# Kernel tuning notes

Hardware: AMD Instinct MI355X
Metric: run time of the kernel (lower is better)

Reference implementation:

```python
import jax, jax.numpy as jnp
import numpy as np

B, M, K, E, V, HOPS = 256, 128, 4, 512, 32000, 3


def setup_inputs() -> dict:
    key = jax.random.key(0)
    ks = jax.random.split(key, 12)

    def emb_table(k):
        t = 0.1 * jax.random.normal(k, (V, E), dtype=jnp.float32)
        return t.at[0].set(0.0)  # padding_idx=0

    inp = {
        "context": jax.random.randint(ks[0], (B, M, K), 0, V),
        "y_": jax.random.randint(ks[1], (B,), 0, V),
        "h_": jax.random.normal(ks[2], (1, B, E), dtype=jnp.float32),
        # embedding tables; C[i] tied to A[i+1], so distinct: A0,A1,A2,C2
        "A0": emb_table(ks[3]),
        "A1": emb_table(ks[4]),
        "A2": emb_table(ks[5]),
        "C2": emb_table(ks[6]),
        # GRU (single layer, single step): PyTorch layout [3E, E] and [3E]
        "W_ih": 0.05 * jax.random.normal(ks[7], (3 * E, E), dtype=jnp.float32),
        "W_hh": 0.05 * jax.random.normal(ks[8], (3 * E, E), dtype=jnp.float32),
        "b_ih": jnp.zeros((3 * E,), dtype=jnp.float32),
        "b_hh": jnp.zeros((3 * E,), dtype=jnp.float32),
        # lin_vocab: Linear(2E -> V)
        "lin_W": 0.02 * jax.random.normal(ks[9], (V, 2 * E), dtype=jnp.float32),
        "lin_b": jnp.zeros((V,), dtype=jnp.float32),
    }
    return inp


def _gru_step(x, h, W_ih, W_hh, b_ih, b_hh):
    gi = x @ W_ih.T + b_ih  # [B, 3E]
    gh = h @ W_hh.T + b_hh
    i_r, i_z, i_n = jnp.split(gi, 3, axis=-1)
    h_r, h_z, h_n = jnp.split(gh, 3, axis=-1)
    r = jax.nn.sigmoid(i_r + h_r)
    z = jax.nn.sigmoid(i_z + h_z)
    n = jnp.tanh(i_n + r * h_n)
    return (1.0 - z) * n + z * h


def reference(context, y_, h_, A0, A1, A2, C2, W_ih, W_hh, b_ih, b_hh, lin_W, lin_b):
    # memories[hop] = sum_k A[hop][context], memories[hops] = sum_k C[hops-1][context]
    tables = [A0, A1, A2, C2]
    memories = [t[context].sum(axis=2) for t in tables]  # each [B, M, E]

    m = A1[y_]  # C[0](y_) -- C[0].weight tied to A[1].weight, [B, E]
    h = _gru_step(m, h_[0], W_ih, W_hh, b_ih, b_hh)  # [B, E]

    q = h
    p = None
    p_vocab = None
    for hop in range(HOPS):
        p = jnp.einsum("bme,be->bm", memories[hop], q)  # dot-attention scores
        attn = jax.nn.softmax(p, axis=1)
        o = jnp.einsum("bm,bme->be", attn, memories[hop + 1])
        if hop == 0:
            p_vocab = jnp.concatenate([q, o], axis=1) @ lin_W.T + lin_b  # [B, V]
        q = q + o

    p_ptr = p  # last hop's pre-softmax scores [B, M]
    return (p_ptr, p_vocab, h[None])  # h: [1, B, E]
```

## Files before the change

kernel.cpp:

```cpp
#include <hip/hip_runtime.h>
#include <hip/hip_bf16.h>
#include <stdint.h>
#include <stddef.h>

#define Bb 256
#define Mm 128
#define Ee 512
#define Vv 32000
#define E3 1536

typedef __attribute__((ext_vector_type(8))) short bf16x8;
typedef __attribute__((ext_vector_type(4))) float f32x4;

__device__ __forceinline__ float bf2f(unsigned short u) {
  union { unsigned int i; float f; } v; v.i = ((unsigned int)u) << 16; return v.f;
}
__device__ __forceinline__ unsigned int f2bf(float f) {
  union { float f; unsigned int u; } v; v.f = f;
  unsigned int u = v.u;
  return ((u + 0x7fffu + ((u >> 16) & 1u)) >> 16);
}

__global__ void convert_kernel(const float* __restrict__ A0, const float* __restrict__ A1,
                               const float* __restrict__ A2,
                               unsigned short* __restrict__ tabB) {
  const int t = blockIdx.y;
  const float* src = (t == 0) ? A0 : (t == 1) ? A1 : A2;
  unsigned short* dst = tabB + (size_t)t * Vv * Ee;
  const int n4 = Vv * Ee / 4;
  for (int i = blockIdx.x * blockDim.x + threadIdx.x; i < n4; i += gridDim.x * blockDim.x) {
    f32x4 v = __builtin_nontemporal_load((const f32x4*)src + i);
    unsigned int o0 = f2bf(v.x) | (f2bf(v.y) << 16);
    unsigned int o1 = f2bf(v.z) | (f2bf(v.w) << 16);
    ((uint2*)dst)[i] = make_uint2(o0, o1);
  }
}

__global__ void gru_gemm_kernel(const int* __restrict__ y,
                                const float* __restrict__ A1,
                                const float* __restrict__ hprev,
                                const float* __restrict__ W_ih,
                                const float* __restrict__ W_hh,
                                float* __restrict__ gi,
                                float* __restrict__ gh) {
  const int z = blockIdx.z;
  const float* W = z ? W_hh : W_ih;
  float* C = z ? gh : gi;
  const int by = blockIdx.x * 64;
  const int jy = blockIdx.y * 64;
  __shared__ float As[16][65];
  __shared__ float Bs[16][65];
  const int tx = threadIdx.x & 15, ty = threadIdx.x >> 4;
  float acc[4][4] = {};
  for (int k0 = 0; k0 < Ee; k0 += 16) {
#pragma unroll
    for (int it = 0; it < 4; ++it) {
      int r = ty + it * 16;
      int row = by + r;
      const float* arow = z ? (hprev + (size_t)row * Ee) : (A1 + (size_t)y[row] * Ee);
      As[tx][r] = arow[k0 + tx];
      Bs[tx][r] = W[(size_t)(jy + r) * Ee + k0 + tx];
    }
    __syncthreads();
#pragma unroll
    for (int kk = 0; kk < 16; ++kk) {
      float a[4], bb[4];
#pragma unroll
      for (int i = 0; i < 4; ++i) { a[i] = As[kk][ty * 4 + i]; bb[i] = Bs[kk][tx * 4 + i]; }
#pragma unroll
      for (int i = 0; i < 4; ++i)
#pragma unroll
        for (int j = 0; j < 4; ++j)
          acc[i][j] += a[i] * bb[j];
    }
    __syncthreads();
  }
#pragma unroll
  for (int i = 0; i < 4; ++i)
#pragma unroll
    for (int j = 0; j < 4; ++j)
      C[(size_t)(by + ty * 4 + i) * E3 + jy + tx * 4 + j] = acc[i][j];
}

__global__ __launch_bounds__(1024) void fused_kernel(
    const int* __restrict__ ctx,
    const unsigned short* __restrict__ tabB,
    const float* __restrict__ A0, const float* __restrict__ A1,
    const float* __restrict__ A2,
    const float* __restrict__ gi, const float* __restrict__ gh,
    const float* __restrict__ b_ih, const float* __restrict__ b_hh,
    const float* __restrict__ h0,
    float* __restrict__ out_h, unsigned short* __restrict__ in2,
    float* __restrict__ p_out) {
  extern __shared__ char smem[];
  unsigned short* Vlds = (unsigned short*)smem;
  float* p_lds = (float*)(smem + 131072);
  float* qbuf = (float*)(smem + 131584);
  float* obuf = (float*)(smem + 133632);

  const int b = blockIdx.x;
  const int tid = threadIdx.x;
  const int lane = tid & 63, w = tid >> 6;

  if (tid < 512) {
    const int e = tid;
    const float* gib = gi + (size_t)b * E3;
    const float* ghb = gh + (size_t)b * E3;
    float ir = gib[e] + b_ih[e];
    float iz = gib[512 + e] + b_ih[512 + e];
    float inn = gib[1024 + e] + b_ih[1024 + e];
    float hr = ghb[e] + b_hh[e];
    float hz = ghb[512 + e] + b_hh[512 + e];
    float hn = ghb[1024 + e] + b_hh[1024 + e];
    float r = 1.f / (1.f + __expf(-(ir + hr)));
    float z = 1.f / (1.f + __expf(-(iz + hz)));
    float n = tanhf(inn + r * hn);
    float hp = h0[(size_t)b * Ee + e];
    float hnew = (1.f - z) * n + z * hp;
    out_h[(size_t)b * Ee + e] = hnew;
    in2[(size_t)b * 1024 + e] = (unsigned short)f2bf(hnew);
    qbuf[e] = hnew;
  }

#define GATHER_B(T)                                                          \
  {                                                                          \
    const unsigned short* Tb = tabB + (size_t)(T) * ((size_t)Vv * Ee);       \
    _Pragma("unroll 2")                                                      \
    for (int r8 = 0; r8 < 8; ++r8) {                                         \
      const int row = w * 8 + r8;                                            \
      const int4 cc = *(const int4*)(ctx + ((size_t)b * Mm + row) * 4);      \
      uint4 va = *(const uint4*)(Tb + (size_t)cc.x * Ee + lane * 8);         \
      uint4 vb = *(const uint4*)(Tb + (size_t)cc.y * Ee + lane * 8);         \
      uint4 vc = *(const uint4*)(Tb + (size_t)cc.z * Ee + lane * 8);         \
      uint4 vd = *(const uint4*)(Tb + (size_t)cc.w * Ee + lane * 8);         \
      const unsigned int* pa = (const unsigned int*)&va;                     \
      const unsigned int* pb = (const unsigned int*)&vb;                     \
      const unsigned int* pc = (const unsigned int*)&vc;                     \
      const unsigned int* pd = (const unsigned int*)&vd;                     \
      unsigned int o[4];                                                     \
      _Pragma("unroll")                                                      \
      for (int j = 0; j < 4; ++j) {                                          \
        float lo = bf2f((unsigned short)(pa[j] & 0xffff)) +                  \
                   bf2f((unsigned short)(pb[j] & 0xffff)) +                  \
                   bf2f((unsigned short)(pc[j] & 0xffff)) +                  \
                   bf2f((unsigned short)(pd[j] & 0xffff));                   \
        float hi = bf2f((unsigned short)(pa[j] >> 16)) +                     \
                   bf2f((unsigned short)(pb[j] >> 16)) +                     \
                   bf2f((unsigned short)(pc[j] >> 16)) +                     \
                   bf2f((unsigned short)(pd[j] >> 16));                      \
        o[j] = f2bf(lo) | (f2bf(hi) << 16);                                  \
      }                                                                      \
      *(uint4*)(Vlds + (size_t)row * Ee + lane * 8) = *(uint4*)o;            \
    }                                                                        \
  }

#define GATHER_F(TAB)                                                        \
  {                                                                          \
    _Pragma("unroll 2")                                                      \
    for (int r8 = 0; r8 < 8; ++r8) {                                         \
      const int row = w * 8 + r8;                                            \
      const int4 cc = *(const int4*)(ctx + ((size_t)b * Mm + row) * 4);      \
      const float* s0 = TAB + (size_t)cc.x * Ee + lane * 8;                  \
      const float* s1 = TAB + (size_t)cc.y * Ee + lane * 8;                  \
      const float* s2 = TAB + (size_t)cc.z * Ee + lane * 8;                  \
      const float* s3 = TAB + (size_t)cc.w * Ee + lane * 8;                  \
      float4 a0 = *(const float4*)s0, a1 = *(const float4*)(s0 + 4);         \
      float4 b0 = *(const float4*)s1, b1 = *(const float4*)(s1 + 4);         \
      float4 c0 = *(const float4*)s2, c1 = *(const float4*)(s2 + 4);         \
      float4 d0 = *(const float4*)s3, d1 = *(const float4*)(s3 + 4);         \
      unsigned int o[4];                                                     \
      o[0] = f2bf(a0.x + b0.x + c0.x + d0.x) |                               \
             (f2bf(a0.y + b0.y + c0.y + d0.y) << 16);                        \
      o[1] = f2bf(a0.z + b0.z + c0.z + d0.z) |                               \
             (f2bf(a0.w + b0.w + c0.w + d0.w) << 16);                        \
      o[2] = f2bf(a1.x + b1.x + c1.x + d1.x) |                               \
             (f2bf(a1.y + b1.y + c1.y + d1.y) << 16);                        \
      o[3] = f2bf(a1.z + b1.z + c1.z + d1.z) |                               \
             (f2bf(a1.w + b1.w + c1.w + d1.w) << 16);                        \
      *(uint4*)(Vlds + (size_t)row * Ee + lane * 8) = *(uint4*)o;            \
    }                                                                        \
  }

#define GATHER(T, TAB) { if (tabB) GATHER_B(T) else GATHER_F(TAB) }

#define SCORE_PHASE(EMIT)                                                    \
  {                                                                          \
    float qf[8];                                                             \
    *(float4*)&qf[0] = *(const float4*)&qbuf[lane * 8];                      \
    *(float4*)&qf[4] = *(const float4*)&qbuf[lane * 8 + 4];                  \
    _Pragma("unroll")                                                        \
    for (int r = 0; r < 8; ++r) {                                            \
      const int m = w * 8 + r;                                               \
      uint4 kv = *(const uint4*)(Vlds + (size_t)m * Ee + lane * 8);          \
      const unsigned int* p4 = (const unsigned int*)&kv;                     \
      float s = 0.f;                                                         \
      _Pragma("unroll")                                                      \
      for (int x = 0; x < 4; ++x) {                                          \
        s += bf2f((unsigned short)(p4[x] & 0xffff)) * qf[2 * x];             \
        s += bf2f((unsigned short)(p4[x] >> 16)) * qf[2 * x + 1];            \
      }                                                                      \
      _Pragma("unroll")                                                      \
      for (int off = 32; off > 0; off >>= 1) s += __shfl_down(s, off);       \
      if (lane == 0) { EMIT; }                                               \
    }                                                                        \
  }

#define SOFTMAX_PHASE                                                        \
  if (tid < 64) {                                                            \
    float v0 = p_lds[tid], v1 = p_lds[tid + 64];                             \
    float mx = fmaxf(v0, v1);                                                \
    _Pragma("unroll")                                                        \
    for (int off = 32; off > 0; off >>= 1) mx = fmaxf(mx, __shfl_xor(mx, off)); \
    float e0 = __expf(v0 - mx), e1 = __expf(v1 - mx);                        \
    float s = e0 + e1;                                                       \
    _Pragma("unroll")                                                        \
    for (int off = 32; off > 0; off >>= 1) s += __shfl_xor(s, off);          \
    float inv = 1.f / s;                                                     \
    p_lds[tid] = e0 * inv;                                                   \
    p_lds[tid + 64] = e1 * inv;                                              \
  }

#define O_PHASE                                                              \
  {                                                                          \
    const int g = tid >> 8, t = tid & 255;                                   \
    const int e2 = t * 2;                                                    \
    float a0 = 0.f, a1 = 0.f;                                                \
    _Pragma("unroll 4")                                                      \
    for (int m = g * 32; m < g * 32 + 32; ++m) {                             \
      unsigned int vv = *(const unsigned int*)(Vlds + (size_t)m * Ee + e2);  \
      float ww = p_lds[m];                                                   \
      a0 += ww * bf2f((unsigned short)(vv & 0xffff));                        \
      a1 += ww * bf2f((unsigned short)(vv >> 16));                           \
    }                                                                        \
    obuf[g * 512 + e2] = a0;                                                 \
    obuf[g * 512 + e2 + 1] = a1;                                             \
  }

  GATHER(0, A0)
  __syncthreads();
  SCORE_PHASE(p_lds[m] = s)
  __syncthreads();
  SOFTMAX_PHASE
  GATHER(1, A1)
  __syncthreads();
  O_PHASE
  __syncthreads();
  if (tid < 512) {
    const int e = tid;
    float o = obuf[e] + obuf[512 + e] + obuf[1024 + e] + obuf[1536 + e];
    qbuf[e] = qbuf[e] + o;
    in2[(size_t)b * 1024 + 512 + e] = (unsigned short)f2bf(o);
  }
  __syncthreads();

  SCORE_PHASE(p_lds[m] = s)
  __syncthreads();
  SOFTMAX_PHASE
  GATHER(2, A2)
  __syncthreads();
  O_PHASE
  __syncthreads();
  if (tid < 512) {
    const int e = tid;
    qbuf[e] = qbuf[e] + obuf[e] + obuf[512 + e] + obuf[1024 + e] + obuf[1536 + e];
  }
  __syncthreads();

  SCORE_PHASE(p_out[b * Mm + m] = s)
}

__global__ __launch_bounds__(512) void pvocab_kernel(
    const unsigned short* __restrict__ in2,
    const float* __restrict__ lin_W,
    const float* __restrict__ lin_b,
    float* __restrict__ out_pv) {
  const int v0 = blockIdx.x * 128;
  const int m0 = blockIdx.y * 128;
  const int tid = threadIdx.x;
  const int lane = tid & 63, w = tid >> 6;
  const int wm = w >> 2, wn = w & 3;
  const int l15 = lane & 15, lg = lane >> 4;
  __shared__ __align__(16) unsigned short As[2][128][64];
  __shared__ __align__(16) unsigned short Ws[2][128][64];

  const int au = tid & 7, arb = tid >> 3;
  const int wc = tid & 15, wrb = tid >> 4;

  f32x4 acc[4][2];
#pragma unroll
  for (int i = 0; i < 4; ++i)
#pragma unroll
    for (int j = 0; j < 2; ++j)
      acc[i][j] = (f32x4){0.f, 0.f, 0.f, 0.f};

  uint4 aR[2];
  float4 wR[4];

#define PV_STAGE_LOAD(K0)                                                    \
  {                                                                          \
    _Pragma("unroll")                                                        \
    for (int it = 0; it < 2; ++it) {                                         \
      int r = arb + it * 64;                                                 \
      aR[it] = *(const uint4*)(in2 + (size_t)(m0 + r) * 1024 + (K0) + au * 8); \
    }                                                                        \
    _Pragma("unroll")                                                        \
    for (int it = 0; it < 4; ++it) {                                         \
      int r = wrb + it * 32;                                                 \
      wR[it] = *(const float4*)(lin_W + (size_t)(v0 + r) * 1024 + (K0) + wc * 4); \
    }                                                                        \
  }

#define PV_STAGE_WRITE(BUF)                                                  \
  {                                                                          \
    _Pragma("unroll")                                                        \
    for (int it = 0; it < 2; ++it) {                                         \
      int r = arb + it * 64;                                                 \
      *(uint4*)(&As[BUF][r][((au + r) & 7) * 8]) = aR[it];                   \
    }                                                                        \
    _Pragma("unroll")                                                        \
    for (int it = 0; it < 4; ++it) {                                         \
      int r = wrb + it * 32;                                                 \
      unsigned int o0 = f2bf(wR[it].x) | (f2bf(wR[it].y) << 16);             \
      unsigned int o1 = f2bf(wR[it].z) | (f2bf(wR[it].w) << 16);             \
      int u = wc >> 1, h = wc & 1;                                           \
      *(uint2*)(&Ws[BUF][r][((u + r) & 7) * 8 + h * 4]) = make_uint2(o0, o1); \
    }                                                                        \
  }

  PV_STAGE_LOAD(0)
  PV_STAGE_WRITE(0)
  __syncthreads();

  int cur = 0;
  for (int t = 0; t < 16; ++t) {
    if (t + 1 < 16) PV_STAGE_LOAD((t + 1) * 64)
#pragma unroll
    for (int kk = 0; kk < 2; ++kk) {
      const int cu = kk * 4 + lg;
      bf16x8 wf[2], af[4];
#pragma unroll
      for (int j = 0; j < 2; ++j) {
        int row = wn * 32 + j * 16 + l15;
        wf[j] = *(const bf16x8*)(&Ws[cur][row][((cu + row) & 7) * 8]);
      }
#pragma unroll
      for (int i = 0; i < 4; ++i) {
        int row = wm * 64 + i * 16 + l15;
        af[i] = *(const bf16x8*)(&As[cur][row][((cu + row) & 7) * 8]);
      }
#pragma unroll
      for (int i = 0; i < 4; ++i)
#pragma unroll
        for (int j = 0; j < 2; ++j)
          acc[i][j] = __builtin_amdgcn_mfma_f32_16x16x32_bf16(af[i], wf[j], acc[i][j], 0, 0, 0);
    }
    if (t + 1 < 16) {
      PV_STAGE_WRITE(cur ^ 1)
      __syncthreads();
      cur ^= 1;
    }
  }

#pragma unroll
  for (int j = 0; j < 2; ++j) {
    int v = v0 + wn * 32 + j * 16 + l15;
    float bias = lin_b[v];
#pragma unroll
    for (int i = 0; i < 4; ++i) {
      int brow = m0 + wm * 64 + i * 16 + lg * 4;
#pragma unroll
      for (int rr = 0; rr < 4; ++rr)
        out_pv[(size_t)(brow + rr) * Vv + v] = acc[i][j][rr] + bias;
    }
  }
}

extern "C" void kernel_launch(void* const* d_in, const int* in_sizes, int n_in,
                              void* d_out, int out_size, void* d_ws, size_t ws_size,
                              hipStream_t stream) {
  const int* ctx = (const int*)d_in[0];
  const int* y = (const int*)d_in[1];
  const float* h0 = (const float*)d_in[2];
  const float* A0 = (const float*)d_in[3];
  const float* A1 = (const float*)d_in[4];
  const float* A2 = (const float*)d_in[5];
  const float* W_ih = (const float*)d_in[7];
  const float* W_hh = (const float*)d_in[8];
  const float* b_ih = (const float*)d_in[9];
  const float* b_hh = (const float*)d_in[10];
  const float* lin_W = (const float*)d_in[11];
  const float* lin_b = (const float*)d_in[12];

  const size_t tabBytes = (size_t)3 * Vv * Ee * 2;
  const size_t giBytes = (size_t)Bb * E3 * 4;
  const size_t in2Bytes = (size_t)Bb * 1024 * 2;
  const bool bf16path = ws_size >= tabBytes + 2 * giBytes + in2Bytes;

  char* ws = (char*)d_ws;
  size_t off = 0;
  unsigned short* tabB = nullptr;
  if (bf16path) { tabB = (unsigned short*)ws; off += tabBytes; }
  float* gi = (float*)(ws + off); off += giBytes;
  float* gh = (float*)(ws + off); off += giBytes;
  unsigned short* in2 = (unsigned short*)(ws + off);

  float* out = (float*)d_out;
  float* p_ptr = out;
  float* p_voc = out + Bb * Mm;
  float* out_h = out + Bb * Mm + (size_t)Bb * Vv;

  if (bf16path)
    convert_kernel<<<dim3(4096, 3), 256, 0, stream>>>(A0, A1, A2, tabB);
  gru_gemm_kernel<<<dim3(4, 24, 2), 256, 0, stream>>>(y, A1, h0, W_ih, W_hh, gi, gh);
  hipFuncSetAttribute((const void*)fused_kernel,
                      hipFuncAttributeMaxDynamicSharedMemorySize, 141824);
  fused_kernel<<<Bb, 1024, 141824, stream>>>(ctx, tabB, A0, A1, A2, gi, gh,
                                             b_ih, b_hh, h0, out_h, in2, p_ptr);
  pvocab_kernel<<<dim3(Vv / 128, 2), 512, 0, stream>>>(in2, lin_W, lin_b, p_voc);
}
```

Baseline: 220.4 us.

## Retile p_vocab GEMM to 64-row blocks with A fragments read from global

Restructures the vocabulary projection kernel into 256-thread blocks covering 64 batch rows by 128 vocab columns, with the batch dimension on grid x so neighbouring blocks share the same lin_W tile through cache. The activation operand is no longer staged in shared memory; each wave loads its bf16 MFMA fragments straight from global memory. Only the converted weight tile is double-buffered in LDS. This cuts LDS use and staging work and gives more blocks, but lin_W is now read and converted by four blocks instead of two, and the uncoalesced global A-fragment loads inside the MFMA loop may add latency.

Result: slower. 348.1 us (+57.9%).

```diff
diff --git a/kernel.cpp b/kernel.cpp
--- a/kernel.cpp
+++ b/kernel.cpp
@@ -269,21 +269,19 @@
   SCORE_PHASE(p_out[b * Mm + m] = s)
 }
 
-__global__ __launch_bounds__(512) void pvocab_kernel(
+__global__ __launch_bounds__(256) void pvocab_kernel(
     const unsigned short* __restrict__ in2,
     const float* __restrict__ lin_W,
     const float* __restrict__ lin_b,
     float* __restrict__ out_pv) {
-  const int v0 = blockIdx.x * 128;
-  const int m0 = blockIdx.y * 128;
+  const int m0 = blockIdx.x * 64;
+  const int v0 = blockIdx.y * 128;
   const int tid = threadIdx.x;
-  const int lane = tid & 63, w = tid >> 6;
-  const int wm = w >> 2, wn = w & 3;
+  const int lane = tid & 63, wn = tid >> 6;
   const int l15 = lane & 15, lg = lane >> 4;
-  __shared__ __align__(16) unsigned short As[2][128][64];
+  const int n_base = v0 + wn * 32;
   __shared__ __align__(16) unsigned short Ws[2][128][64];
 
-  const int au = tid & 7, arb = tid >> 3;
   const int wc = tid & 15, wrb = tid >> 4;
 
   f32x4 acc[4][2];
@@ -293,33 +291,22 @@
     for (int j = 0; j < 2; ++j)
       acc[i][j] = (f32x4){0.f, 0.f, 0.f, 0.f};
 
-  uint4 aR[2];
-  float4 wR[4];
+  float4 wR[8];
 
 #define PV_STAGE_LOAD(K0)                                                    \
   {                                                                          \
     _Pragma("unroll")                                                        \
-    for (int it = 0; it < 2; ++it) {                                         \
-      int r = arb + it * 64;                                                 \
-      aR[it] = *(const uint4*)(in2 + (size_t)(m0 + r) * 1024 + (K0) + au * 8); \
-    }                                                                        \
+    for (int it = 0; it < 8; ++it) {                                         \
+      int r = wrb + it * 16;                                                 \
+      wR[it] = *(const float4*)(lin_W + (size_t)(v0 + r) * 1024 + (K0) + wc * 4); \
+    }                                                                        \
+  }
+
+#define PV_STAGE_WRITE(BUF)                                                  \
+  {                                                                          \
     _Pragma("unroll")                                                        \
-    for (int it = 0; it < 4; ++it) {                                         \
-      int r = wrb + it * 32;                                                 \
-      wR[it] = *(const float4*)(lin_W + (size_t)(v0 + r) * 1024 + (K0) + wc * 4); \
-    }                                                                        \
-  }
-
-#define PV_STAGE_WRITE(BUF)                                                  \
-  {                                                                          \
-    _Pragma("unroll")                                                        \
-    for (int it = 0; it < 2; ++it) {                                         \
-      int r = arb + it * 64;                                                 \
-      *(uint4*)(&As[BUF][r][((au + r) & 7) * 8]) = aR[it];                   \
-    }                                                                        \
-    _Pragma("unroll")                                                        \
-    for (int it = 0; it < 4; ++it) {                                         \
-      int r = wrb + it * 32;                                                 \
+    for (int it = 0; it < 8; ++it) {                                         \
+      int r = wrb + it * 16;                                                 \
       unsigned int o0 = f2bf(wR[it].x) | (f2bf(wR[it].y) << 16);             \
       unsigned int o1 = f2bf(wR[it].z) | (f2bf(wR[it].w) << 16);             \
       int u = wc >> 1, h = wc & 1;                                           \
@@ -337,6 +324,7 @@
 #pragma unroll
     for (int kk = 0; kk < 2; ++kk) {
       const int cu = kk * 4 + lg;
+      const int col = t * 64 + kk * 32 + lg * 8;
       bf16x8 wf[2], af[4];
 #pragma unroll
       for (int j = 0; j < 2; ++j) {
@@ -344,10 +332,8 @@
         wf[j] = *(const bf16x8*)(&Ws[cur][row][((cu + row) & 7) * 8]);
       }
 #pragma unroll
-      for (int i = 0; i < 4; ++i) {
-        int row = wm * 64 + i * 16 + l15;
-        af[i] = *(const bf16x8*)(&As[cur][row][((cu + row) & 7) * 8]);
-      }
+      for (int i = 0; i < 4; ++i)
+        af[i] = *(const bf16x8*)(in2 + (size_t)(m0 + i * 16 + l15) * 1024 + col);
 #pragma unroll
       for (int i = 0; i < 4; ++i)
 #pragma unroll
@@ -363,11 +349,11 @@
 
 #pragma unroll
   for (int j = 0; j < 2; ++j) {
-    int v = v0 + wn * 32 + j * 16 + l15;
+    int v = n_base + j * 16 + l15;
     float bias = lin_b[v];
 #pragma unroll
     for (int i = 0; i < 4; ++i) {
-      int brow = m0 + wm * 64 + i * 16 + lg * 4;
+      int brow = m0 + i * 16 + lg * 4;
 #pragma unroll
       for (int rr = 0; rr < 4; ++rr)
         out_pv[(size_t)(brow + rr) * Vv + v] = acc[i][j][rr] + bias;
@@ -416,5 +402,5 @@
                       hipFuncAttributeMaxDynamicSharedMemorySize, 141824);
   fused_kernel<<<Bb, 1024, 141824, stream>>>(ctx, tabB, A0, A1, A2, gi, gh,
                                              b_ih, b_hh, h0, out_h, in2, p_ptr);
-  pvocab_kernel<<<dim3(Vv / 128, 2), 512, 0, stream>>>(in2, lin_W, lin_b, p_voc);
-}
+  pvocab_kernel<<<dim3(4, Vv / 128), 256, 0, stream>>>(in2, lin_W, lin_b, p_voc);
+}
```

## Store activations in MFMA fragment layout and cover full batch per vocab tile

Applied to the files above, without the earlier changes.

The fused kernel now writes the bf16 [h, o] activations in a pre-swizzled layout that matches the MFMA A-fragment order. The vocab GEMM can then load A fragments straight from global memory instead of staging them through LDS. Each pvocab block now has 1024 threads and covers all 256 batch rows for its 128 vocab columns, so every lin_W tile is read and converted to bf16 once instead of twice. K-steps are widened to 128, which halves the number of barriers. The cost is per-MFMA global loads of activations, which rely on L2 hits, and fewer blocks (250) for the device's CUs.

New measurement: 218.6 us. No clear change (-0.8%).

```diff
diff --git a/kernel.cpp b/kernel.cpp
--- a/kernel.cpp
+++ b/kernel.cpp
@@ -20,6 +20,10 @@
   unsigned int u = v.u;
   return ((u + 0x7fffu + ((u >> 16) & 1u)) >> 16);
 }
+
+#define IN2F_IDX(bb, col)                                                     \
+  ((((size_t)((bb) >> 4) * 32 + ((col) >> 5)) * 512) +                        \
+   (size_t)((((bb) & 15) + (((col) >> 3) & 3) * 16) * 8 + ((col) & 7)))
 
 __global__ void convert_kernel(const float* __restrict__ A0, const float* __restrict__ A1,
                                const float* __restrict__ A2,
@@ -90,7 +94,7 @@
     const float* __restrict__ gi, const float* __restrict__ gh,
     const float* __restrict__ b_ih, const float* __restrict__ b_hh,
     const float* __restrict__ h0,
-    float* __restrict__ out_h, unsigned short* __restrict__ in2,
+    float* __restrict__ out_h, unsigned short* __restrict__ in2f,
     float* __restrict__ p_out) {
   extern __shared__ char smem[];
   unsigned short* Vlds = (unsigned short*)smem;
@@ -118,7 +122,7 @@
     float hp = h0[(size_t)b * Ee + e];
     float hnew = (1.f - z) * n + z * hp;
     out_h[(size_t)b * Ee + e] = hnew;
-    in2[(size_t)b * 1024 + e] = (unsigned short)f2bf(hnew);
+    in2f[IN2F_IDX(b, e)] = (unsigned short)f2bf(hnew);
     qbuf[e] = hnew;
   }
 
@@ -249,7 +253,7 @@
     const int e = tid;
     float o = obuf[e] + obuf[512 + e] + obuf[1024 + e] + obuf[1536 + e];
     qbuf[e] = qbuf[e] + o;
-    in2[(size_t)b * 1024 + 512 + e] = (unsigned short)f2bf(o);
+    in2f[IN2F_IDX(b, 512 + e)] = (unsigned short)f2bf(o);
   }
   __syncthreads();
 
@@ -269,22 +273,19 @@
   SCORE_PHASE(p_out[b * Mm + m] = s)
 }
 
-__global__ __launch_bounds__(512) void pvocab_kernel(
-    const unsigned short* __restrict__ in2,
+__global__ __launch_bounds__(1024) void pvocab_kernel(
+    const unsigned short* __restrict__ in2f,
     const float* __restrict__ lin_W,
     const float* __restrict__ lin_b,
     float* __restrict__ out_pv) {
   const int v0 = blockIdx.x * 128;
-  const int m0 = blockIdx.y * 128;
   const int tid = threadIdx.x;
   const int lane = tid & 63, w = tid >> 6;
   const int wm = w >> 2, wn = w & 3;
   const int l15 = lane & 15, lg = lane >> 4;
-  __shared__ __align__(16) unsigned short As[2][128][64];
-  __shared__ __align__(16) unsigned short Ws[2][128][64];
-
-  const int au = tid & 7, arb = tid >> 3;
-  const int wc = tid & 15, wrb = tid >> 4;
+  __shared__ __align__(16) unsigned short Ws[2][128][128];
+
+  const int wc = tid & 31, wrb = tid >> 5;
 
   f32x4 acc[4][2];
 #pragma unroll
@@ -293,37 +294,26 @@
     for (int j = 0; j < 2; ++j)
       acc[i][j] = (f32x4){0.f, 0.f, 0.f, 0.f};
 
-  uint4 aR[2];
   float4 wR[4];
 
-#define PV_STAGE_LOAD(K0)                                                    \
-  {                                                                          \
-    _Pragma("unroll")                                                        \
-    for (int it = 0; it < 2; ++it) {                                         \
-      int r = arb + it * 64;                                                 \
-      aR[it] = *(const uint4*)(in2 + (size_t)(m0 + r) * 1024 + (K0) + au * 8); \
-    }                                                                        \
+#define PV_STAGE_LOAD(T)                                                     \
+  {                                                                          \
     _Pragma("unroll")                                                        \
     for (int it = 0; it < 4; ++it) {                                         \
       int r = wrb + it * 32;                                                 \
-      wR[it] = *(const float4*)(lin_W + (size_t)(v0 + r) * 1024 + (K0) + wc * 4); \
+      wR[it] = *(const float4*)(lin_W + (size_t)(v0 + r) * 1024 + (T) * 128 + wc * 4); \
     }                                                                        \
   }
 
 #define PV_STAGE_WRITE(BUF)                                                  \
   {                                                                          \
-    _Pragma("unroll")                                                        \
-    for (int it = 0; it < 2; ++it) {                                         \
-      int r = arb + it * 64;                                                 \
-      *(uint4*)(&As[BUF][r][((au + r) & 7) * 8]) = aR[it];                   \
-    }                                                                        \
     _Pragma("unroll")                                                        \
     for (int it = 0; it < 4; ++it) {                                         \
       int r = wrb + it * 32;                                                 \
       unsigned int o0 = f2bf(wR[it].x) | (f2bf(wR[it].y) << 16);             \
       unsigned int o1 = f2bf(wR[it].z) | (f2bf(wR[it].w) << 16);             \
       int u = wc >> 1, h = wc & 1;                                           \
-      *(uint2*)(&Ws[BUF][r][((u + r) & 7) * 8 + h * 4]) = make_uint2(o0, o1); \
+      *(uint2*)(&Ws[BUF][r][((u + r) & 15) * 8 + h * 4]) = make_uint2(o0, o1); \
     }                                                                        \
   }
 
@@ -332,21 +322,21 @@
   __syncthreads();
 
   int cur = 0;
-  for (int t = 0; t < 16; ++t) {
-    if (t + 1 < 16) PV_STAGE_LOAD((t + 1) * 64)
-#pragma unroll
-    for (int kk = 0; kk < 2; ++kk) {
-      const int cu = kk * 4 + lg;
+  for (int t = 0; t < 8; ++t) {
+    if (t + 1 < 8) PV_STAGE_LOAD(t + 1)
+#pragma unroll
+    for (int kb4 = 0; kb4 < 4; ++kb4) {
+      const int kb = t * 4 + kb4;
       bf16x8 wf[2], af[4];
 #pragma unroll
       for (int j = 0; j < 2; ++j) {
         int row = wn * 32 + j * 16 + l15;
-        wf[j] = *(const bf16x8*)(&Ws[cur][row][((cu + row) & 7) * 8]);
+        wf[j] = *(const bf16x8*)(&Ws[cur][row][((kb4 * 4 + lg + row) & 15) * 8]);
       }
 #pragma unroll
       for (int i = 0; i < 4; ++i) {
-        int row = wm * 64 + i * 16 + l15;
-        af[i] = *(const bf16x8*)(&As[cur][row][((cu + row) & 7) * 8]);
+        int mblk = wm * 4 + i;
+        af[i] = *(const bf16x8*)(in2f + ((size_t)(mblk * 32 + kb)) * 512 + lane * 8);
       }
 #pragma unroll
       for (int i = 0; i < 4; ++i)
@@ -354,7 +344,7 @@
         for (int j = 0; j < 2; ++j)
           acc[i][j] = __builtin_amdgcn_mfma_f32_16x16x32_bf16(af[i], wf[j], acc[i][j], 0, 0, 0);
     }
-    if (t + 1 < 16) {
+    if (t + 1 < 8) {
       PV_STAGE_WRITE(cur ^ 1)
       __syncthreads();
       cur ^= 1;
@@ -367,7 +357,7 @@
     float bias = lin_b[v];
 #pragma unroll
     for (int i = 0; i < 4; ++i) {
-      int brow = m0 + wm * 64 + i * 16 + lg * 4;
+      int brow = wm * 64 + i * 16 + lg * 4;
 #pragma unroll
       for (int rr = 0; rr < 4; ++rr)
         out_pv[(size_t)(brow + rr) * Vv + v] = acc[i][j][rr] + bias;
@@ -402,7 +392,7 @@
   if (bf16path) { tabB = (unsigned short*)ws; off += tabBytes; }
   float* gi = (float*)(ws + off); off += giBytes;
   float* gh = (float*)(ws + off); off += giBytes;
-  unsigned short* in2 = (unsigned short*)(ws + off);
+  unsigned short* in2f = (unsigned short*)(ws + off);
 
   float* out = (float*)d_out;
   float* p_ptr = out;
@@ -415,6 +405,6 @@
   hipFuncSetAttribute((const void*)fused_kernel,
                       hipFuncAttributeMaxDynamicSharedMemorySize, 141824);
   fused_kernel<<<Bb, 1024, 141824, stream>>>(ctx, tabB, A0, A1, A2, gi, gh,
-                                             b_ih, b_hh, h0, out_h, in2, p_ptr);
-  pvocab_kernel<<<dim3(Vv / 128, 2), 512, 0, stream>>>(in2, lin_W, lin_b, p_voc);
-}
+                                             b_ih, b_hh, h0, out_h, in2f, p_ptr);
+  pvocab_kernel<<<Vv / 128, 1024, 0, stream>>>(in2f, lin_W, lin_b, p_voc);
+}
```
